# Kernel optimization log

Hardware: AMD Instinct MI355X
Metric: run time of the kernel (lower is better)

Reference implementation:

```python
import jax, jax.numpy as jnp
import numpy as np

BETA = 0.25  # commitment weight from __init__ default
K, D = 512, 64


def setup_inputs() -> dict:
    key = jax.random.key(0)
    k1, k2 = jax.random.split(key)
    latents = jax.random.normal(k1, (32, 64, 64, 64), dtype=jnp.float32)  # [B, D, H, W]
    # nn.Embedding weight initialized uniform(-1/K, 1/K)
    emb_weight = jax.random.uniform(k2, (K, D), dtype=jnp.float32, minval=-1.0 / K, maxval=1.0 / K)
    return {"latents": latents, "emb_weight": emb_weight, "validation": 1}


def reference(latents, emb_weight, validation):
    B, Dc, H, W = latents.shape
    lat = jnp.transpose(latents, (0, 2, 3, 1))          # [B, H, W, D]
    flat = lat.reshape(-1, Dc)                           # [N, D]
    # pairwise squared distances via sum-of-squares + matmul (as in source)
    dist = (jnp.sum(flat * flat, axis=1, keepdims=True)
            + jnp.sum(emb_weight * emb_weight, axis=1)
            - 2.0 * flat @ emb_weight.T)                 # [N, K]
    inds = jnp.argmin(dist, axis=1)                      # [N]
    # one_hot @ emb_weight == gather
    q = emb_weight[inds].reshape(B, H, W, Dc)            # [B, H, W, D]
    commitment_loss = jnp.mean((jax.lax.stop_gradient(q) - lat) ** 2)
    embedding_loss = jnp.mean((q - jax.lax.stop_gradient(lat)) ** 2)
    # eloss starts at 0.0 (and stays 0 in validation), so topology terms vanish
    vq_loss = commitment_loss * BETA + embedding_loss
    # straight-through estimator
    q_st = lat + jax.lax.stop_gradient(q - lat)
    return jnp.transpose(q_st, (0, 3, 1, 2)), vq_loss
```

## Files before the change

### kernel.cpp

```cpp
#include <hip/hip_runtime.h>


typedef __bf16 bf16_t;
typedef __attribute__((ext_vector_type(8))) __bf16 bf16x8;
typedef __attribute__((ext_vector_type(16))) float floatx16;

namespace {
constexpr int K    = 512;
constexpr int D    = 64;
constexpr int HW   = 4096;
constexpr int NPIX = 32 * HW;
constexpr int QOUT = NPIX * D;
constexpr int DEXT = 80;
constexpr int G    = 2;
}

__global__ __launch_bounds__(64) void vq_prep(const float* __restrict__ emb,
                                              bf16_t* __restrict__ ext,
                                              float* __restrict__ loss) {
    int k = blockIdx.x * 64 + threadIdx.x;
    if (k == 0) *loss = 0.0f;
    if (k >= K) return;
    const float4* row = (const float4*)(emb + k * D);
    float4 v[16];
#pragma unroll
    for (int i = 0; i < 16; ++i) v[i] = row[i];
    float s = 0.0f;
#pragma unroll
    for (int i = 0; i < 16; ++i)
        s += v[i].x * v[i].x + v[i].y * v[i].y + v[i].z * v[i].z + v[i].w * v[i].w;
    bf16_t r[DEXT];
#pragma unroll
    for (int i = 0; i < 16; ++i) {
        r[4 * i + 0] = (bf16_t)v[i].x;
        r[4 * i + 1] = (bf16_t)v[i].y;
        r[4 * i + 2] = (bf16_t)v[i].z;
        r[4 * i + 3] = (bf16_t)v[i].w;
    }
    r[64] = (bf16_t)(-0.5f * s);
#pragma unroll
    for (int i = 65; i < DEXT; ++i) r[i] = (bf16_t)0.0f;
#pragma unroll
    for (int i = 0; i < DEXT / 8; ++i)
        ((bf16x8*)(ext + k * DEXT))[i] = *(const bf16x8*)(r + 8 * i);
}

__global__ __launch_bounds__(256) void vq_mfma(
    const float* __restrict__ lat,
    const float* __restrict__ emb,
    const bf16_t* __restrict__ ext,
    float* __restrict__ out,
    float* __restrict__ loss) {
    const int lane = threadIdx.x & 63;
    const int wave = threadIdx.x >> 6;
    const int col  = lane & 31;
    const int half = lane >> 5;
    const int nb   = blockIdx.x * (64 * G * 4) / 2 + wave * 64;

    int bg[G], hwg[G];
    bf16x8 bfrag[G][5];
#pragma unroll
    for (int g = 0; g < G; ++g) {
        int n = nb + g * 32 + col;
        bg[g] = n >> 12;
        hwg[g] = n & (HW - 1);
        const float* latp = lat + (size_t)bg[g] * D * HW + hwg[g];
#pragma unroll
        for (int s = 0; s < 4; ++s) {
#pragma unroll
            for (int j = 0; j < 8; ++j) {
                int d = s * 16 + half * 8 + j;
                bfrag[g][s][j] = (bf16_t)latp[(size_t)d * HW];
            }
        }
#pragma unroll
        for (int j = 0; j < 8; ++j) bfrag[g][4][j] = (bf16_t)0.0f;
        if (half == 0) bfrag[g][4][0] = (bf16_t)1.0f;
    }

    float best[G];
    int   bestk[G];
#pragma unroll
    for (int g = 0; g < G; ++g) { best[g] = -3.4e38f; bestk[g] = 0; }

#pragma unroll 4
    for (int t = 0; t < 16; ++t) {
        const bf16_t* arow = ext + ((size_t)(t * 32 + col)) * DEXT + half * 8;
        bf16x8 af[5];
#pragma unroll
        for (int s = 0; s < 5; ++s) af[s] = *(const bf16x8*)(arow + s * 16);

        floatx16 acc[G];
#pragma unroll
        for (int g = 0; g < G; ++g) {
#pragma unroll
            for (int r = 0; r < 16; ++r) acc[g][r] = 0.0f;
#pragma unroll
            for (int s = 0; s < 5; ++s)
                acc[g] = __builtin_amdgcn_mfma_f32_32x32x16_bf16(
                    af[s], bfrag[g][s], acc[g], 0, 0, 0);
        }
#pragma unroll
        for (int g = 0; g < G; ++g) {
#pragma unroll
            for (int r = 0; r < 16; ++r) {
                if (acc[g][r] > best[g]) {
                    best[g]  = acc[g][r];
                    bestk[g] = t * 32 + (r & 3) + 8 * (r >> 2) + 4 * half;
                }
            }
        }
    }

    float sqtot = 0.0f;
#pragma unroll
    for (int g = 0; g < G; ++g) {
        float ob  = __shfl_xor(best[g], 32, 64);
        int   obk = __shfl_xor(bestk[g], 32, 64);
        if (ob > best[g] || (ob == best[g] && obk < bestk[g])) {
            best[g] = ob; bestk[g] = obk;
        }

        const float* eb = emb + bestk[g] * D + half * 8;
        float* outp     = out + (size_t)bg[g] * D * HW + hwg[g];
        float sq = 0.0f;
#pragma unroll
        for (int s = 0; s < 4; ++s) {
            float4 q0 = *(const float4*)(eb + s * 16);
            float4 q1 = *(const float4*)(eb + s * 16 + 4);
            float x0 = (float)bfrag[g][s][0], x1 = (float)bfrag[g][s][1];
            float x2 = (float)bfrag[g][s][2], x3 = (float)bfrag[g][s][3];
            float x4 = (float)bfrag[g][s][4], x5 = (float)bfrag[g][s][5];
            float x6 = (float)bfrag[g][s][6], x7 = (float)bfrag[g][s][7];
            float d0 = q0.x - x0, d1 = q0.y - x1, d2 = q0.z - x2, d3 = q0.w - x3;
            float d4 = q1.x - x4, d5 = q1.y - x5, d6 = q1.z - x6, d7 = q1.w - x7;
            sq += d0 * d0 + d1 * d1 + d2 * d2 + d3 * d3;
            sq += d4 * d4 + d5 * d5 + d6 * d6 + d7 * d7;
            const int dbase = s * 16 + half * 8;
            outp[(size_t)(dbase + 0) * HW] = q0.x;
            outp[(size_t)(dbase + 1) * HW] = q0.y;
            outp[(size_t)(dbase + 2) * HW] = q0.z;
            outp[(size_t)(dbase + 3) * HW] = q0.w;
            outp[(size_t)(dbase + 4) * HW] = q1.x;
            outp[(size_t)(dbase + 5) * HW] = q1.y;
            outp[(size_t)(dbase + 6) * HW] = q1.z;
            outp[(size_t)(dbase + 7) * HW] = q1.w;
        }
        sqtot += sq;
    }

#pragma unroll
    for (int off = 32; off > 0; off >>= 1) sqtot += __shfl_down(sqtot, off, 64);
    __shared__ float part[4];
    if (lane == 0) part[wave] = sqtot;
    __syncthreads();
    if (threadIdx.x == 0) {
        float t = part[0] + part[1] + part[2] + part[3];
        atomicAdd(loss, t * (1.25f / (float)QOUT));
    }
}

extern "C" void kernel_launch(void* const* d_in, const int* in_sizes, int n_in,
                              void* d_out, int out_size, void* d_ws, size_t ws_size,
                              hipStream_t stream) {
    const float* lat = (const float*)d_in[0];
    const float* emb = (const float*)d_in[1];
    float* out       = (float*)d_out;
    float* loss      = out + QOUT;
    bf16_t* ext      = (bf16_t*)d_ws;

    vq_prep<<<K / 64, 64, 0, stream>>>(emb, ext, loss);
    vq_mfma<<<NPIX / 256, 256, 0, stream>>>(lat, emb, ext, out, loss);
}
```

Baseline: 109.2 us.

## Pair adjacent pixels per lane and pack argmax index into float bits

Each lane now handles two adjacent pixels, so latent loads and quantized-output stores become float2 accesses instead of scalar strided ones. The argmin over codes is rewritten as an unsigned max over a packed key: the accumulator is biased by 1.0, the low 9 mantissa bits are replaced by the code index, and a single integer max replaces the compare-and-select pair. This cuts VALU work in the inner loop and the number of memory instructions. The cost is score precision: truncating mantissa bits can change which code wins near-ties, ties now go to the higher index, and the bias assumes scores stay positive.

```diff
diff --git a/kernel.cpp b/kernel.cpp
--- a/kernel.cpp
+++ b/kernel.cpp
@@ -12,7 +12,6 @@
 constexpr int NPIX = 32 * HW;
 constexpr int QOUT = NPIX * D;
 constexpr int DEXT = 80;
-constexpr int G    = 2;
 }
 
 __global__ __launch_bounds__(64) void vq_prep(const float* __restrict__ emb,
@@ -55,33 +54,36 @@
     const int wave = threadIdx.x >> 6;
     const int col  = lane & 31;
     const int half = lane >> 5;
-    const int nb   = blockIdx.x * (64 * G * 4) / 2 + wave * 64;
+    const unsigned h4 = (unsigned)(half << 2);
+    const int nb   = blockIdx.x * 256 + wave * 64;
 
-    int bg[G], hwg[G];
-    bf16x8 bfrag[G][5];
+    const int n0 = nb + 2 * col;
+    const int b  = n0 >> 12;
+    const int hw = n0 & (HW - 1);
+    const float* latp = lat + (size_t)b * D * HW + hw;
+
+    bf16x8 bfrag[2][5];
 #pragma unroll
-    for (int g = 0; g < G; ++g) {
-        int n = nb + g * 32 + col;
-        bg[g] = n >> 12;
-        hwg[g] = n & (HW - 1);
-        const float* latp = lat + (size_t)bg[g] * D * HW + hwg[g];
+    for (int s = 0; s < 4; ++s) {
 #pragma unroll
-        for (int s = 0; s < 4; ++s) {
+        for (int j = 0; j < 8; ++j) {
+            int d = s * 16 + half * 8 + j;
+            float2 v = *(const float2*)(latp + (size_t)d * HW);
+            bfrag[0][s][j] = (bf16_t)v.x;
+            bfrag[1][s][j] = (bf16_t)v.y;
+        }
+    }
 #pragma unroll
-            for (int j = 0; j < 8; ++j) {
-                int d = s * 16 + half * 8 + j;
-                bfrag[g][s][j] = (bf16_t)latp[(size_t)d * HW];
-            }
-        }
-#pragma unroll
-        for (int j = 0; j < 8; ++j) bfrag[g][4][j] = (bf16_t)0.0f;
-        if (half == 0) bfrag[g][4][0] = (bf16_t)1.0f;
+    for (int j = 0; j < 8; ++j) {
+        bfrag[0][4][j] = (bf16_t)0.0f;
+        bfrag[1][4][j] = (bf16_t)0.0f;
+    }
+    if (half == 0) {
+        bfrag[0][4][0] = (bf16_t)1.0f;
+        bfrag[1][4][0] = (bf16_t)1.0f;
     }
 
-    float best[G];
-    int   bestk[G];
-#pragma unroll
-    for (int g = 0; g < G; ++g) { best[g] = -3.4e38f; bestk[g] = 0; }
+    unsigned best0 = 0u, best1 = 0u;
 
 #pragma unroll 4
     for (int t = 0; t < 16; ++t) {
@@ -90,63 +92,57 @@
 #pragma unroll
         for (int s = 0; s < 5; ++s) af[s] = *(const bf16x8*)(arow + s * 16);
 
-        floatx16 acc[G];
+        floatx16 acc0, acc1;
 #pragma unroll
-        for (int g = 0; g < G; ++g) {
+        for (int r = 0; r < 16; ++r) { acc0[r] = 1.0f; acc1[r] = 1.0f; }
 #pragma unroll
-            for (int r = 0; r < 16; ++r) acc[g][r] = 0.0f;
+        for (int s = 0; s < 5; ++s)
+            acc0 = __builtin_amdgcn_mfma_f32_32x32x16_bf16(af[s], bfrag[0][s], acc0, 0, 0, 0);
 #pragma unroll
-            for (int s = 0; s < 5; ++s)
-                acc[g] = __builtin_amdgcn_mfma_f32_32x32x16_bf16(
-                    af[s], bfrag[g][s], acc[g], 0, 0, 0);
-        }
+        for (int s = 0; s < 5; ++s)
+            acc1 = __builtin_amdgcn_mfma_f32_32x32x16_bf16(af[s], bfrag[1][s], acc1, 0, 0, 0);
+
 #pragma unroll
-        for (int g = 0; g < G; ++g) {
-#pragma unroll
-            for (int r = 0; r < 16; ++r) {
-                if (acc[g][r] > best[g]) {
-                    best[g]  = acc[g][r];
-                    bestk[g] = t * 32 + (r & 3) + 8 * (r >> 2) + 4 * half;
-                }
-            }
+        for (int r = 0; r < 16; ++r) {
+            unsigned codebase = (unsigned)(t * 32 + ((r & 3) + 8 * (r >> 2)));
+            unsigned c0 = (__float_as_uint(acc0[r]) & 0xFFFFFE00u) | codebase | h4;
+            unsigned c1 = (__float_as_uint(acc1[r]) & 0xFFFFFE00u) | codebase | h4;
+            best0 = best0 > c0 ? best0 : c0;
+            best1 = best1 > c1 ? best1 : c1;
         }
     }
 
+    {
+        unsigned o0 = (unsigned)__shfl_xor((int)best0, 32, 64);
+        unsigned o1 = (unsigned)__shfl_xor((int)best1, 32, 64);
+        best0 = best0 > o0 ? best0 : o0;
+        best1 = best1 > o1 ? best1 : o1;
+    }
+    const int k0 = (int)(best0 & 511u);
+    const int k1 = (int)(best1 & 511u);
+
+    const float* e0 = emb + k0 * D + half * 8;
+    const float* e1 = emb + k1 * D + half * 8;
+    float* outp = out + (size_t)b * D * HW + hw;
     float sqtot = 0.0f;
 #pragma unroll
-    for (int g = 0; g < G; ++g) {
-        float ob  = __shfl_xor(best[g], 32, 64);
-        int   obk = __shfl_xor(bestk[g], 32, 64);
-        if (ob > best[g] || (ob == best[g] && obk < bestk[g])) {
-            best[g] = ob; bestk[g] = obk;
+    for (int s = 0; s < 4; ++s) {
+        float4 a0 = *(const float4*)(e0 + s * 16);
+        float4 a1 = *(const float4*)(e0 + s * 16 + 4);
+        float4 c0 = *(const float4*)(e1 + s * 16);
+        float4 c1 = *(const float4*)(e1 + s * 16 + 4);
+        float q0[8] = {a0.x, a0.y, a0.z, a0.w, a1.x, a1.y, a1.z, a1.w};
+        float q1[8] = {c0.x, c0.y, c0.z, c0.w, c1.x, c1.y, c1.z, c1.w};
+#pragma unroll
+        for (int j = 0; j < 8; ++j) {
+            float x0 = (float)bfrag[0][s][j];
+            float x1 = (float)bfrag[1][s][j];
+            float d0 = q0[j] - x0;
+            float d1 = q1[j] - x1;
+            sqtot += d0 * d0 + d1 * d1;
+            int d = s * 16 + half * 8 + j;
+            *(float2*)(outp + (size_t)d * HW) = make_float2(q0[j], q1[j]);
         }
-
-        const float* eb = emb + bestk[g] * D + half * 8;
-        float* outp     = out + (size_t)bg[g] * D * HW + hwg[g];
-        float sq = 0.0f;
-#pragma unroll
-        for (int s = 0; s < 4; ++s) {
-            float4 q0 = *(const float4*)(eb + s * 16);
-            float4 q1 = *(const float4*)(eb + s * 16 + 4);
-            float x0 = (float)bfrag[g][s][0], x1 = (float)bfrag[g][s][1];
-            float x2 = (float)bfrag[g][s][2], x3 = (float)bfrag[g][s][3];
-            float x4 = (float)bfrag[g][s][4], x5 = (float)bfrag[g][s][5];
-            float x6 = (float)bfrag[g][s][6], x7 = (float)bfrag[g][s][7];
-            float d0 = q0.x - x0, d1 = q0.y - x1, d2 = q0.z - x2, d3 = q0.w - x3;
-            float d4 = q1.x - x4, d5 = q1.y - x5, d6 = q1.z - x6, d7 = q1.w - x7;
-            sq += d0 * d0 + d1 * d1 + d2 * d2 + d3 * d3;
-            sq += d4 * d4 + d5 * d5 + d6 * d6 + d7 * d7;
-            const int dbase = s * 16 + half * 8;
-            outp[(size_t)(dbase + 0) * HW] = q0.x;
-            outp[(size_t)(dbase + 1) * HW] = q0.y;
-            outp[(size_t)(dbase + 2) * HW] = q0.z;
-            outp[(size_t)(dbase + 3) * HW] = q0.w;
-            outp[(size_t)(dbase + 4) * HW] = q1.x;
-            outp[(size_t)(dbase + 5) * HW] = q1.y;
-            outp[(size_t)(dbase + 6) * HW] = q1.z;
-            outp[(size_t)(dbase + 7) * HW] = q1.w;
-        }
-        sqtot += sq;
     }
 
 #pragma unroll
```

Result: faster. 106.6 us (-2.4%).
